# Performance work log

Hardware: AMD Instinct MI355X
Metric: run time of the kernel (lower is better)

## Reference

```python
import jax, jax.numpy as jnp
import numpy as np

N = 7          # N_AGENTS (hardcoded in source)
H = 4          # n_heads
TOP_K = 3
EPS = 1e-5
NEG = -1.0e9


def _gat(x, W, a_src, a_dst, edge_mask):
    # x: (B,N,F), W: (F,H*Hd), a_src/a_dst: (H,Hd), edge_mask: (N,N)
    B = x.shape[0]
    Hd = a_src.shape[1]
    h = (x @ W).reshape(B, N, H, Hd)
    s_src = jnp.einsum('bnhd,hd->bnh', h, a_src)
    s_dst = jnp.einsum('bnhd,hd->bnh', h, a_dst)
    e = s_src[:, :, None, :] + s_dst[:, None, :, :]          # (B,N,N,H)
    e = jnp.where(e > 0, e, 0.2 * e)                          # LeakyReLU(0.2)
    m = edge_mask[None, :, :, None]
    e = e * m + (1.0 - m) * NEG
    if TOP_K < N:
        # k-th largest along axis=2 (ascending sort -> index N-TOP_K)
        thr = jnp.sort(e, axis=2)[:, :, N - TOP_K:N - TOP_K + 1, :]
        sm = (e >= thr).astype(e.dtype)
        e = e * sm + (1.0 - sm) * NEG
    alpha = jax.nn.softmax(e, axis=2)
    alpha = jnp.nan_to_num(alpha)
    out = jnp.einsum('bijh,bjhd->bihd', alpha, h).reshape(B, N, H * Hd)
    return out, alpha.mean(-1)


def _ln(x, w, b):
    mu = x.mean(-1, keepdims=True)
    var = ((x - mu) ** 2).mean(-1, keepdims=True)
    return (x - mu) / jnp.sqrt(var + EPS) * w + b


def _forward(node_feats, context, base_preds, regime_feats, edge_logits,
             W1, a_src1, a_dst1, W2, a_src2, a_dst2,
             ln1_w, ln1_b, ln2_w, ln2_b, skip_w, skip_b,
             base_w1, base_b1, base_w2, base_b2,
             reg_w1, reg_b1, reg_w2, reg_b2,
             gate_w1, gate_b1, gate_w2, gate_b2,
             res_w1, res_b1, res_w2, res_b2):
    B = node_feats.shape[0]
    eye = jnp.eye(N, dtype=edge_logits.dtype)
    edge_mask = jax.nn.sigmoid(edge_logits) * (1.0 - eye) + eye

    skip = node_feats @ skip_w + skip_b
    h1, _ = _gat(node_feats, W1, a_src1, a_dst1, edge_mask)
    h = jax.nn.relu(_ln(h1 + skip, ln1_w, ln1_b))
    h2, attn = _gat(h, W2, a_src2, a_dst2, edge_mask)
    h = jax.nn.relu(_ln(h2 + h, ln2_w, ln2_b))

    combined = jnp.concatenate([h.reshape(B, -1), context], axis=-1)
    w_base = jax.nn.softmax(jax.nn.relu(combined @ base_w1 + base_b1) @ base_w2 + base_b2, axis=-1)
    w_regime = jax.nn.softmax(jax.nn.relu(combined @ reg_w1 + reg_b1) @ reg_w2 + reg_b2, axis=-1)
    gate = jax.nn.sigmoid(jnp.tanh(regime_feats @ gate_w1 + gate_b1) @ gate_w2 + gate_b2)  # (B,1)
    weights = (1.0 - gate) * w_base + gate * w_regime
    pred = (weights * base_preds).sum(-1)
    residual = (jnp.tanh(combined @ res_w1 + res_b1) @ res_w2 + res_b2)[:, 0] * 0.05
    pred = jnp.maximum(pred + residual, 0.05)
    return pred, weights, gate, edge_mask, attn


def setup_inputs() -> dict:
    key = jax.random.key(0)
    B, F, C, HID, NB = 16384, 256, 128, 256, 2
    Hd = HID // H
    G = N * HID + C
    ks = iter(jax.random.split(key, 40))
    nrm = lambda shp, s: jax.random.normal(next(ks), shp, jnp.float32) * s
    d = {
        'node_feats': nrm((B, N, F), 1.0),
        'context': nrm((B, C), 1.0),
        'base_preds': jax.random.uniform(next(ks), (B, NB), jnp.float32),
        'regime_feats': nrm((B, 3), 1.0),
        'edge_logits': nrm((N, N), 0.1),
        'W1': nrm((F, HID), (2.0 / (F + HID)) ** 0.5),
        'a_src1': nrm((H, Hd), 0.1), 'a_dst1': nrm((H, Hd), 0.1),
        'W2': nrm((HID, HID), (1.0 / HID) ** 0.5),
        'a_src2': nrm((H, Hd), 0.1), 'a_dst2': nrm((H, Hd), 0.1),
        'ln1_w': jnp.ones((HID,), jnp.float32), 'ln1_b': jnp.zeros((HID,), jnp.float32),
        'ln2_w': jnp.ones((HID,), jnp.float32), 'ln2_b': jnp.zeros((HID,), jnp.float32),
        'skip_w': nrm((F, HID), (1.0 / F) ** 0.5), 'skip_b': jnp.zeros((HID,), jnp.float32),
        'base_w1': nrm((G, 32), (1.0 / G) ** 0.5), 'base_b1': jnp.zeros((32,), jnp.float32),
        'base_w2': nrm((32, NB), 0.1), 'base_b2': jnp.zeros((NB,), jnp.float32),
        'reg_w1': nrm((G, 32), (1.0 / G) ** 0.5), 'reg_b1': jnp.zeros((32,), jnp.float32),
        'reg_w2': nrm((32, NB), 0.1), 'reg_b2': jnp.zeros((NB,), jnp.float32),
        'gate_w1': nrm((3, 8), 0.5), 'gate_b1': jnp.zeros((8,), jnp.float32),
        'gate_w2': nrm((8, 1), 0.3), 'gate_b2': jnp.zeros((1,), jnp.float32),
        'res_w1': nrm((G, 16), (1.0 / G) ** 0.5), 'res_b1': jnp.zeros((16,), jnp.float32),
        'res_w2': nrm((16, 1), 0.2), 'res_b2': jnp.zeros((1,), jnp.float32),
    }
    return d


def reference(node_feats, context, base_preds, regime_feats, edge_logits,
              W1, a_src1, a_dst1, W2, a_src2, a_dst2,
              ln1_w, ln1_b, ln2_w, ln2_b, skip_w, skip_b,
              base_w1, base_b1, base_w2, base_b2,
              reg_w1, reg_b1, reg_w2, reg_b2,
              gate_w1, gate_b1, gate_w2, gate_b2,
              res_w1, res_b1, res_w2, res_b2):
    return _forward(node_feats, context, base_preds, regime_feats, edge_logits,
                    W1, a_src1, a_dst1, W2, a_src2, a_dst2,
                    ln1_w, ln1_b, ln2_w, ln2_b, skip_w, skip_b,
                    base_w1, base_b1, base_w2, base_b2,
                    reg_w1, reg_b1, reg_w2, reg_b2,
                    gate_w1, gate_b1, gate_w2, gate_b2,
                    res_w1, res_b1, res_w2, res_b2)
```

## Files before the change

kernel.cpp:

```cpp
#include <hip/hip_runtime.h>
#include <hip/hip_bf16.h>

typedef unsigned short u16;
typedef __attribute__((ext_vector_type(8))) short bfrag8;
typedef __attribute__((ext_vector_type(8))) unsigned short u16x8;
typedef __attribute__((ext_vector_type(4))) unsigned short u16x4;
typedef __attribute__((ext_vector_type(4))) float f32x4;

__device__ __forceinline__ float bf2f(u16 u) {
    union { unsigned int i; float f; } v; v.i = ((unsigned int)u) << 16; return v.f;
}
__device__ __forceinline__ u16 f2bf(float f) {
    union { __hip_bfloat16 h; u16 u; } cv;
    cv.h = __float2bfloat16(f);
    return cv.u;
}
__device__ __forceinline__ float fast_tanh(float x) {
    float e = __expf(2.f * x);
    return (e - 1.f) / (e + 1.f);
}

#define TILE_M 128
#define TILE_N 128
#define TILE_K 32

#define GLOAD_LDS16(g, l) \
    __builtin_amdgcn_global_load_lds( \
        (const __attribute__((address_space(1))) void*)(g), \
        (__attribute__((address_space(3))) void*)(l), 16, 0, 0)

template<int HAS_BIAS, int C_MODE, int NGUARD>
__global__ __launch_bounds__(256)
void gemm_k(const u16* __restrict__ A, const u16* __restrict__ Bt,
            const float* __restrict__ bias, void* __restrict__ Cp,
            int M, int N, int K, int lda, int ldc, int nt, int kchunk)
{
    __shared__ u16 As[2][TILE_M][TILE_K];
    __shared__ u16 Bs[2][TILE_N][TILE_K];

    const int nwg = gridDim.x;
    const int q = nwg >> 3, r = nwg & 7;
    const int xcd = blockIdx.x & 7, pos = blockIdx.x >> 3;
    const int wg = (xcd < r ? xcd * (q + 1) : r * (q + 1) + (xcd - r) * q) + pos;
    const int m0 = (wg / nt) * TILE_M;
    const int n0 = (wg % nt) * TILE_N;

    const int kc   = blockIdx.y;
    const int kbeg = kc * kchunk;
    const int kend = (kbeg + kchunk < K) ? kbeg + kchunk : K;

    const int t    = threadIdx.x;
    const int lane = t & 63;
    const int w    = t >> 6;
    const int wm   = (w >> 1) * 64;
    const int wn   = (w & 1) * 64;
    const int lr   = lane & 15;
    const int kg   = (lane >> 4) * 8;

    const int lrow = lane >> 2;
    const int lcol = (lane & 3) * 8;
    const u16* gA0 = A  + (size_t)(m0 + 32 * w + lrow) * lda + lcol;
    const u16* gA1 = gA0 + (size_t)16 * lda;
    const u16* gB0 = Bt + (size_t)(n0 + 32 * w + lrow) * K + lcol;
    const u16* gB1 = gB0 + (size_t)16 * K;
    char* lA = (char*)&As[0][0][0] + w * 2048;
    char* lB = (char*)&Bs[0][0][0] + w * 2048;

    f32x4 acc[4][4];
#pragma unroll
    for (int i = 0; i < 4; ++i)
#pragma unroll
        for (int j = 0; j < 4; ++j) acc[i][j] = (f32x4){0.f, 0.f, 0.f, 0.f};

#define ISSUE(bufo, k0v) { \
        GLOAD_LDS16(gA0 + (k0v), lA + (bufo)); \
        GLOAD_LDS16(gA1 + (k0v), lA + 1024 + (bufo)); \
        GLOAD_LDS16(gB0 + (k0v), lB + (bufo)); \
        GLOAD_LDS16(gB1 + (k0v), lB + 1024 + (bufo)); \
    }

    ISSUE(0, kbeg)
    int buf = 0;
    for (int k0 = kbeg; k0 < kend; k0 += TILE_K) {
        const bool more = (k0 + TILE_K) < kend;
        if (more) {
            ISSUE((buf ^ 1) * 8192, k0 + TILE_K);
            asm volatile("s_waitcnt vmcnt(4)" ::: "memory");
        } else {
            asm volatile("s_waitcnt vmcnt(0)" ::: "memory");
        }
        __syncthreads();

        bfrag8 af[4], bfr[4];
#pragma unroll
        for (int mi = 0; mi < 4; ++mi) af[mi]  = *(const bfrag8*)&As[buf][wm + mi * 16 + lr][kg];
#pragma unroll
        for (int ni = 0; ni < 4; ++ni) bfr[ni] = *(const bfrag8*)&Bs[buf][wn + ni * 16 + lr][kg];
#pragma unroll
        for (int mi = 0; mi < 4; ++mi)
#pragma unroll
            for (int ni = 0; ni < 4; ++ni)
                acc[mi][ni] = __builtin_amdgcn_mfma_f32_16x16x32_bf16(af[mi], bfr[ni], acc[mi][ni], 0, 0, 0);

        __syncthreads();
        buf ^= 1;
    }
#undef ISSUE

    float* Cf = (float*)Cp + (size_t)kc * M * ldc;
#pragma unroll
    for (int mi = 0; mi < 4; ++mi) {
#pragma unroll
        for (int ni = 0; ni < 4; ++ni) {
            int col = n0 + wn + ni * 16 + lr;
            if (!NGUARD || col < N) {
                int row = m0 + wm + mi * 16 + (lane >> 4) * 4;
                float bv = 0.f;
                if (HAS_BIAS && kc == 0) bv = bias[col];
#pragma unroll
                for (int rr = 0; rr < 4; ++rr) {
                    float v = acc[mi][ni][rr] + bv;
                    if (C_MODE == 0) ((u16*)Cp)[(size_t)(row + rr) * ldc + col] = f2bf(v);
                    else             Cf[(size_t)(row + rr) * ldc + col] = v;
                }
            }
        }
    }
}

__global__ __launch_bounds__(256)
void precast_k(const float* __restrict__ in, u16* __restrict__ out, int n8)
{
    int i = blockIdx.x * 256 + threadIdx.x;
    if (i >= n8) return;
    const float4* p = (const float4*)(in + (size_t)i * 8);
    float4 a = p[0], b = p[1];
    u16x8 v;
    v[0] = f2bf(a.x); v[1] = f2bf(a.y); v[2] = f2bf(a.z); v[3] = f2bf(a.w);
    v[4] = f2bf(b.x); v[5] = f2bf(b.y); v[6] = f2bf(b.z); v[7] = f2bf(b.w);
    *(u16x8*)(out + (size_t)i * 8) = v;
}

__global__ __launch_bounds__(256)
void score_k(const u16* __restrict__ hs, int ld,
             const float* __restrict__ a_src, const float* __restrict__ a_dst,
             float* __restrict__ scores, int Mrows)
{
    const int wid  = blockIdx.x * 4 + (threadIdx.x >> 6);
    const int lane = threadIdx.x & 63;
    if (wid >= Mrows) return;
    const u16* hp = hs + (size_t)wid * ld + lane * 4;
    u16x4 xv = *(const u16x4*)hp;
    float s1 = 0.f, s2 = 0.f;
#pragma unroll
    for (int k = 0; k < 4; ++k) {
        float x = bf2f(xv[k]);
        s1 = fmaf(x, a_src[lane * 4 + k], s1);
        s2 = fmaf(x, a_dst[lane * 4 + k], s2);
    }
#pragma unroll
    for (int off = 1; off < 16; off <<= 1) {
        s1 += __shfl_xor(s1, off);
        s2 += __shfl_xor(s2, off);
    }
    if ((lane & 15) == 0) {
        scores[(size_t)wid * 8 + (lane >> 4)] = s1;
        scores[(size_t)wid * 8 + 4 + (lane >> 4)] = s2;
    }
}

template<int WRITE_ATTN>
__global__ __launch_bounds__(256)
void alpha_k(const float* __restrict__ scores, const float* __restrict__ em2,
             float* __restrict__ alpha, float* __restrict__ attn_out)
{
    const int t = blockIdx.x * 256 + threadIdx.x;
    const int b = t >> 2;
    const int h = t & 3;

    float ssrc[7], sdst[7];
#pragma unroll
    for (int n = 0; n < 7; ++n) {
        ssrc[n] = scores[(size_t)(b * 7 + n) * 8 + h];
        sdst[n] = scores[(size_t)(b * 7 + n) * 8 + 4 + h];
    }

    float al[49];
#pragma unroll
    for (int i = 0; i < 7; ++i) {
        float e[7];
#pragma unroll
        for (int j = 0; j < 7; ++j) {
            float v = ssrc[i] + sdst[j];
            v = fmaxf(v, 0.2f * v);
            e[j] = fmaf(v, em2[(i * 7 + j) * 2], em2[(i * 7 + j) * 2 + 1]);
        }
        float a1 = -3e38f, b1 = -3e38f, c1 = -3e38f;
#pragma unroll
        for (int j = 0; j < 7; ++j) {
            float v = e[j];
            float t2 = fminf(a1, v); a1 = fmaxf(a1, v);
            float t3 = fminf(b1, t2); b1 = fmaxf(b1, t2);
            c1 = fmaxf(c1, t3);
        }
        float psum = 0.f;
        float p[7];
#pragma unroll
        for (int j = 0; j < 7; ++j) {
            float qv = (e[j] >= c1) ? __expf(e[j] - a1) : 0.f;
            p[j] = qv; psum += qv;
        }
        float inv = 1.f / psum;
#pragma unroll
        for (int j = 0; j < 7; ++j) al[i * 7 + j] = p[j] * inv;
    }

    float* ap = alpha + (size_t)t * 49;
#pragma unroll
    for (int j = 0; j < 49; ++j) ap[j] = al[j];

    if (WRITE_ATTN) {
#pragma unroll
        for (int j = 0; j < 49; ++j) {
            float m = al[j];
            m += __shfl_xor(m, 1);
            m += __shfl_xor(m, 2);
            if (h == 0) attn_out[(size_t)b * 49 + j] = 0.25f * m;
        }
    }
}

__global__ __launch_bounds__(256)
void gat_apply_k(const u16* __restrict__ hh, int ld_hh,
                 const u16* __restrict__ resid, int ld_res, int res_off,
                 const float* __restrict__ alpha,
                 const float* __restrict__ ln_w, const float* __restrict__ ln_b,
                 u16* __restrict__ outp, int out_bs)
{
    const int t = threadIdx.x;
    const int b = blockIdx.x * 4 + (t >> 6);
    const int l = t & 63;
    const int c = l * 4;
    const int h = l >> 4;
    const size_t rowbase = (size_t)b * 7;

    float hv[7][4];
#pragma unroll
    for (int n = 0; n < 7; ++n) {
        u16x4 qv = *(const u16x4*)&hh[(rowbase + n) * ld_hh + c];
#pragma unroll
        for (int k = 0; k < 4; ++k) hv[n][k] = bf2f(qv[k]);
    }

    const float* ap = alpha + ((size_t)b * 4 + h) * 49;
    float4 lw = *(const float4*)&ln_w[c];
    float4 lb = *(const float4*)&ln_b[c];

#pragma unroll
    for (int i = 0; i < 7; ++i) {
        float a0 = ap[i * 7 + 0], a1 = ap[i * 7 + 1], a2 = ap[i * 7 + 2],
              a3 = ap[i * 7 + 3], a4 = ap[i * 7 + 4], a5 = ap[i * 7 + 5],
              a6 = ap[i * 7 + 6];
        u16x4 rr = *(const u16x4*)&resid[(rowbase + i) * ld_res + res_off + c];
        float x[4];
#pragma unroll
        for (int k = 0; k < 4; ++k) {
            float pv = a0 * hv[0][k];
            pv = fmaf(a1, hv[1][k], pv);
            pv = fmaf(a2, hv[2][k], pv);
            pv = fmaf(a3, hv[3][k], pv);
            pv = fmaf(a4, hv[4][k], pv);
            pv = fmaf(a5, hv[5][k], pv);
            pv = fmaf(a6, hv[6][k], pv);
            x[k] = pv + bf2f(rr[k]);
        }
        float s1 = (x[0] + x[1]) + (x[2] + x[3]);
        float s2 = fmaf(x[0], x[0], x[1] * x[1]) + fmaf(x[2], x[2], x[3] * x[3]);
#pragma unroll
        for (int off = 32; off > 0; off >>= 1) {
            s1 += __shfl_xor(s1, off);
            s2 += __shfl_xor(s2, off);
        }
        float mu  = s1 * (1.f / 256.f);
        float var = fmaxf(s2 * (1.f / 256.f) - mu * mu, 0.f);
        float inv = rsqrtf(var + 1e-5f);
        u16x4 o;
        o[0] = f2bf(fmaxf((x[0] - mu) * inv * lw.x + lb.x, 0.f));
        o[1] = f2bf(fmaxf((x[1] - mu) * inv * lw.y + lb.y, 0.f));
        o[2] = f2bf(fmaxf((x[2] - mu) * inv * lw.z + lb.z, 0.f));
        o[3] = f2bf(fmaxf((x[3] - mu) * inv * lw.w + lb.w, 0.f));
        *(u16x4*)&outp[(size_t)b * out_bs + i * 256 + c] = o;
    }
}

__global__ __launch_bounds__(256)
void prep_k(const float* __restrict__ W1, const float* __restrict__ skip_w, const float* __restrict__ W2,
            const float* __restrict__ base_w1, const float* __restrict__ reg_w1, const float* __restrict__ res_w1,
            const float* __restrict__ skip_b, const float* __restrict__ base_b1, const float* __restrict__ reg_b1,
            const float* __restrict__ res_b1, const float* __restrict__ edge_logits,
            u16* __restrict__ Wt1, u16* __restrict__ Wt2, u16* __restrict__ Wt3,
            float* __restrict__ bias1, float* __restrict__ bias3,
            float* __restrict__ em2, float* __restrict__ em_out)
{
    int idx = blockIdx.x * 256 + threadIdx.x;
    if (idx < 512 * 256) {
        int n = idx >> 8, k = idx & 255;
        float v = (n < 256) ? W1[k * 256 + n] : skip_w[k * 256 + (n - 256)];
        Wt1[n * 256 + k] = f2bf(v); return;
    }
    idx -= 512 * 256;
    if (idx < 256 * 256) {
        int n = idx >> 8, k = idx & 255;
        Wt2[n * 256 + k] = f2bf(W2[k * 256 + n]); return;
    }
    idx -= 256 * 256;
    if (idx < 128 * 1920) {
        int n = idx / 1920, k = idx % 1920;
        float v = (n < 32) ? base_w1[k * 32 + n]
                : (n < 64) ? reg_w1[k * 32 + (n - 32)]
                : (n < 80) ? res_w1[k * 16 + (n - 64)] : 0.f;
        Wt3[n * 1920 + k] = f2bf(v); return;
    }
    idx -= 128 * 1920;
    if (idx < 512) { bias1[idx] = (idx < 256) ? 0.f : skip_b[idx - 256]; return; }
    idx -= 512;
    if (idx < 80) {
        bias3[idx] = (idx < 32) ? base_b1[idx] : (idx < 64) ? reg_b1[idx - 32] : res_b1[idx - 64];
        return;
    }
    idx -= 80;
    if (idx < 49) {
        int i = idx / 7, j = idx % 7;
        float s = 1.f / (1.f + __expf(-edge_logits[idx]));
        float m = (i == j) ? 1.f : s;
        em2[idx * 2] = m;
        em2[idx * 2 + 1] = (1.f - m) * (-1e9f);
        em_out[idx] = m;
    }
}

__global__ __launch_bounds__(256)
void ctx_k(const float* __restrict__ ctx, u16* __restrict__ comb)
{
    int idx = blockIdx.x * 256 + threadIdx.x;
    int b = idx >> 7, cc = idx & 127;
    comb[(size_t)b * 1920 + 1792 + cc] = f2bf(ctx[idx]);
}

__global__ __launch_bounds__(64)
void head_finish(const float* __restrict__ ho,
                 const float* __restrict__ bp, const float* __restrict__ rf,
                 const float* __restrict__ bw2, const float* __restrict__ bb2,
                 const float* __restrict__ rw2, const float* __restrict__ rb2,
                 const float* __restrict__ gw1, const float* __restrict__ gb1,
                 const float* __restrict__ gw2, const float* __restrict__ gb2,
                 const float* __restrict__ resw2, const float* __restrict__ resb2,
                 float* __restrict__ out_pred, float* __restrict__ out_w, float* __restrict__ out_gate, int B)
{
    int b = blockIdx.x * 64 + threadIdx.x;
    if (b >= B) return;
    const size_t ss = (size_t)B * 80;
    const float* p = ho + (size_t)b * 80;

    float z0 = bb2[0], z1 = bb2[1];
#pragma unroll
    for (int j = 0; j < 32; j += 4) {
        float4 a0 = *(const float4*)(p + j);
        float4 a1 = *(const float4*)(p + ss + j);
        float4 a2 = *(const float4*)(p + 2 * ss + j);
        float4 a3 = *(const float4*)(p + 3 * ss + j);
        float v;
        v = fmaxf((a0.x + a1.x) + (a2.x + a3.x), 0.f); z0 = fmaf(v, bw2[2*j+0], z0); z1 = fmaf(v, bw2[2*j+1], z1);
        v = fmaxf((a0.y + a1.y) + (a2.y + a3.y), 0.f); z0 = fmaf(v, bw2[2*j+2], z0); z1 = fmaf(v, bw2[2*j+3], z1);
        v = fmaxf((a0.z + a1.z) + (a2.z + a3.z), 0.f); z0 = fmaf(v, bw2[2*j+4], z0); z1 = fmaf(v, bw2[2*j+5], z1);
        v = fmaxf((a0.w + a1.w) + (a2.w + a3.w), 0.f); z0 = fmaf(v, bw2[2*j+6], z0); z1 = fmaf(v, bw2[2*j+7], z1);
    }
    float mz = fmaxf(z0, z1); float e0 = __expf(z0 - mz), e1 = __expf(z1 - mz); float inv = 1.f / (e0 + e1);
    float wb0 = e0 * inv, wb1 = e1 * inv;

    z0 = rb2[0]; z1 = rb2[1];
#pragma unroll
    for (int j = 0; j < 32; j += 4) {
        float4 a0 = *(const float4*)(p + 32 + j);
        float4 a1 = *(const float4*)(p + ss + 32 + j);
        float4 a2 = *(const float4*)(p + 2 * ss + 32 + j);
        float4 a3 = *(const float4*)(p + 3 * ss + 32 + j);
        float v;
        v = fmaxf((a0.x + a1.x) + (a2.x + a3.x), 0.f); z0 = fmaf(v, rw2[2*j+0], z0); z1 = fmaf(v, rw2[2*j+1], z1);
        v = fmaxf((a0.y + a1.y) + (a2.y + a3.y), 0.f); z0 = fmaf(v, rw2[2*j+2], z0); z1 = fmaf(v, rw2[2*j+3], z1);
        v = fmaxf((a0.z + a1.z) + (a2.z + a3.z), 0.f); z0 = fmaf(v, rw2[2*j+4], z0); z1 = fmaf(v, rw2[2*j+5], z1);
        v = fmaxf((a0.w + a1.w) + (a2.w + a3.w), 0.f); z0 = fmaf(v, rw2[2*j+6], z0); z1 = fmaf(v, rw2[2*j+7], z1);
    }
    mz = fmaxf(z0, z1); e0 = __expf(z0 - mz); e1 = __expf(z1 - mz); inv = 1.f / (e0 + e1);
    float wr0 = e0 * inv, wr1 = e1 * inv;

    float r = resb2[0];
#pragma unroll
    for (int j = 0; j < 16; j += 4) {
        float4 a0 = *(const float4*)(p + 64 + j);
        float4 a1 = *(const float4*)(p + ss + 64 + j);
        float4 a2 = *(const float4*)(p + 2 * ss + 64 + j);
        float4 a3 = *(const float4*)(p + 3 * ss + 64 + j);
        r = fmaf(fast_tanh((a0.x + a1.x) + (a2.x + a3.x)), resw2[j + 0], r);
        r = fmaf(fast_tanh((a0.y + a1.y) + (a2.y + a3.y)), resw2[j + 1], r);
        r = fmaf(fast_tanh((a0.z + a1.z) + (a2.z + a3.z)), resw2[j + 2], r);
        r = fmaf(fast_tanh((a0.w + a1.w) + (a2.w + a3.w)), resw2[j + 3], r);
    }

    float g = gb2[0];
#pragma unroll
    for (int j = 0; j < 8; ++j) {
        float a = gb1[j];
#pragma unroll
        for (int i = 0; i < 3; ++i) a += rf[(size_t)b * 3 + i] * gw1[i * 8 + j];
        g += fast_tanh(a) * gw2[j];
    }
    float gg = 1.f / (1.f + __expf(-g));
    float w0 = (1.f - gg) * wb0 + gg * wr0;
    float w1 = (1.f - gg) * wb1 + gg * wr1;
    float pred = w0 * bp[(size_t)b * 2] + w1 * bp[(size_t)b * 2 + 1];
    pred = fmaxf(pred + r * 0.05f, 0.05f);
    out_pred[b] = pred;
    out_w[(size_t)b * 2] = w0; out_w[(size_t)b * 2 + 1] = w1;
    out_gate[b] = gg;
}

extern "C" void kernel_launch(void* const* d_in, const int* in_sizes, int n_in,
                              void* d_out, int out_size, void* d_ws, size_t ws_size,
                              hipStream_t stream)
{
    const int B = in_sizes[1] / 128;
    const int Mbig = B * 7;

    const float* node_feats   = (const float*)d_in[0];
    const float* context      = (const float*)d_in[1];
    const float* base_preds   = (const float*)d_in[2];
    const float* regime_feats = (const float*)d_in[3];
    const float* edge_logits  = (const float*)d_in[4];
    const float* W1      = (const float*)d_in[5];
    const float* a_src1  = (const float*)d_in[6];
    const float* a_dst1  = (const float*)d_in[7];
    const float* W2      = (const float*)d_in[8];
    const float* a_src2  = (const float*)d_in[9];
    const float* a_dst2  = (const float*)d_in[10];
    const float* ln1_w   = (const float*)d_in[11];
    const float* ln1_b   = (const float*)d_in[12];
    const float* ln2_w   = (const float*)d_in[13];
    const float* ln2_b   = (const float*)d_in[14];
    const float* skip_w  = (const float*)d_in[15];
    const float* skip_b  = (const float*)d_in[16];
    const float* base_w1 = (const float*)d_in[17];
    const float* base_b1 = (const float*)d_in[18];
    const float* base_w2 = (const float*)d_in[19];
    const float* base_b2 = (const float*)d_in[20];
    const float* reg_w1  = (const float*)d_in[21];
    const float* reg_b1  = (const float*)d_in[22];
    const float* reg_w2  = (const float*)d_in[23];
    const float* reg_b2  = (const float*)d_in[24];
    const float* gate_w1 = (const float*)d_in[25];
    const float* gate_b1 = (const float*)d_in[26];
    const float* gate_w2 = (const float*)d_in[27];
    const float* gate_b2 = (const float*)d_in[28];
    const float* res_w1  = (const float*)d_in[29];
    const float* res_b1  = (const float*)d_in[30];
    const float* res_w2  = (const float*)d_in[31];
    const float* res_b2  = (const float*)d_in[32];

    char* ws = (char*)d_ws;
    size_t off = 0;
    u16* hs1 = (u16*)(ws + off);
    u16* hh2 = (u16*)(ws + off);
    off += (size_t)Mbig * 512 * 2;
    u16* hbuf = (u16*)(ws + off);  off += (size_t)Mbig * 256 * 2;
    u16* comb = (u16*)(ws + off);  off += (size_t)B * 1920 * 2;
    u16* nf_bf = comb;
    float* headout = (float*)(ws + off); off += (size_t)4 * B * 80 * 4;
    u16* Wt1 = (u16*)(ws + off); off += 512 * 256 * 2;
    u16* Wt2 = (u16*)(ws + off); off += 256 * 256 * 2;
    u16* Wt3 = (u16*)(ws + off); off += (size_t)128 * 1920 * 2;
    float* bias1 = (float*)(ws + off); off += 512 * 4;
    float* bias3 = (float*)(ws + off); off += 128 * 4;
    float* em2   = (float*)(ws + off); off += 128 * 4;
    float* scoresb = (float*)(ws + off); off += (size_t)Mbig * 8 * 4;
    float* alphab  = (float*)(ws + off); off += (size_t)B * 4 * 49 * 4;

    float* out_pred = (float*)d_out;
    float* out_w    = out_pred + B;
    float* out_gate = out_pred + 3 * (size_t)B;
    float* out_em   = out_pred + 4 * (size_t)B;
    float* out_attn = out_pred + 4 * (size_t)B + 49;

    const int B4blocks = (B * 4) / 256;

    {
        int n8 = Mbig * 256 / 8;
        precast_k<<<dim3((n8 + 255) / 256), dim3(256), 0, stream>>>(node_feats, nf_bf, n8);
    }

    prep_k<<<dim3(1731), dim3(256), 0, stream>>>(W1, skip_w, W2, base_w1, reg_w1, res_w1,
        skip_b, base_b1, reg_b1, res_b1, edge_logits, Wt1, Wt2, Wt3, bias1, bias3, em2, out_em);

    gemm_k<1, 0, 0><<<dim3((Mbig / 128) * 4, 1), dim3(256), 0, stream>>>(
        nf_bf, Wt1, bias1, (void*)hs1, Mbig, 512, 256, 256, 512, 4, 256);

    score_k<<<dim3(Mbig / 4), dim3(256), 0, stream>>>(hs1, 512, a_src1, a_dst1, scoresb, Mbig);

    alpha_k<0><<<dim3(B4blocks), dim3(256), 0, stream>>>(scoresb, em2, alphab, (float*)nullptr);

    gat_apply_k<<<dim3(B / 4), dim3(256), 0, stream>>>(
        hs1, 512, hs1, 512, 256, alphab, ln1_w, ln1_b, hbuf, 1792);

    gemm_k<0, 0, 0><<<dim3((Mbig / 128) * 2, 1), dim3(256), 0, stream>>>(
        hbuf, Wt2, (const float*)nullptr, (void*)hh2, Mbig, 256, 256, 256, 256, 2, 256);

    score_k<<<dim3(Mbig / 4), dim3(256), 0, stream>>>(hh2, 256, a_src2, a_dst2, scoresb, Mbig);

    alpha_k<1><<<dim3(B4blocks), dim3(256), 0, stream>>>(scoresb, em2, alphab, out_attn);

    gat_apply_k<<<dim3(B / 4), dim3(256), 0, stream>>>(
        hh2, 256, hbuf, 256, 0, alphab, ln2_w, ln2_b, comb, 1920);

    ctx_k<<<dim3(B * 128 / 256), dim3(256), 0, stream>>>(context, comb);

    gemm_k<1, 1, 1><<<dim3(B / 128, 4), dim3(256), 0, stream>>>(
        comb, Wt3, bias3, (void*)headout, B, 80, 1920, 1920, 80, 1, 480);

    head_finish<<<dim3((B + 63) / 64), dim3(64), 0, stream>>>(
        headout, base_preds, regime_feats, base_w2, base_b2, reg_w2, reg_b2,
        gate_w1, gate_b1, gate_w2, gate_b2, res_w2, res_b2, out_pred, out_w, out_gate, B);
}
```

Measured before the change: 289.1 us.

## Replace double-buffered GEMM K loop with single-buffer templated BK tile

```diff
diff --git a/kernel.cpp b/kernel.cpp
--- a/kernel.cpp
+++ b/kernel.cpp
@@ -22,21 +22,20 @@
 
 #define TILE_M 128
 #define TILE_N 128
-#define TILE_K 32
 
 #define GLOAD_LDS16(g, l) \
     __builtin_amdgcn_global_load_lds( \
         (const __attribute__((address_space(1))) void*)(g), \
         (__attribute__((address_space(3))) void*)(l), 16, 0, 0)
 
-template<int HAS_BIAS, int C_MODE, int NGUARD>
+template<int BK, int HAS_BIAS, int C_MODE, int NGUARD>
 __global__ __launch_bounds__(256)
 void gemm_k(const u16* __restrict__ A, const u16* __restrict__ Bt,
             const float* __restrict__ bias, void* __restrict__ Cp,
             int M, int N, int K, int lda, int ldc, int nt, int kchunk)
 {
-    __shared__ u16 As[2][TILE_M][TILE_K];
-    __shared__ u16 Bs[2][TILE_N][TILE_K];
+    __shared__ u16 As[TILE_M][BK];
+    __shared__ u16 Bs[TILE_N][BK];
 
     const int nwg = gridDim.x;
     const int q = nwg >> 3, r = nwg & 7;
@@ -57,14 +56,15 @@
     const int lr   = lane & 15;
     const int kg   = (lane >> 4) * 8;
 
-    const int lrow = lane >> 2;
-    const int lcol = (lane & 3) * 8;
-    const u16* gA0 = A  + (size_t)(m0 + 32 * w + lrow) * lda + lcol;
-    const u16* gA1 = gA0 + (size_t)16 * lda;
-    const u16* gB0 = Bt + (size_t)(n0 + 32 * w + lrow) * K + lcol;
-    const u16* gB1 = gB0 + (size_t)16 * K;
-    char* lA = (char*)&As[0][0][0] + w * 2048;
-    char* lB = (char*)&Bs[0][0][0] + w * 2048;
+    constexpr int ISSUES = BK / 16;
+
+    int irow[ISSUES], icol[ISSUES];
+#pragma unroll
+    for (int j = 0; j < ISSUES; ++j) {
+        int off = j * 4096 + t * 16;
+        irow[j] = off / (2 * BK);
+        icol[j] = (off & (2 * BK - 1)) >> 1;
+    }
 
     f32x4 acc[4][4];
 #pragma unroll
@@ -72,40 +72,33 @@
 #pragma unroll
         for (int j = 0; j < 4; ++j) acc[i][j] = (f32x4){0.f, 0.f, 0.f, 0.f};
 
-#define ISSUE(bufo, k0v) { \
-        GLOAD_LDS16(gA0 + (k0v), lA + (bufo)); \
-        GLOAD_LDS16(gA1 + (k0v), lA + 1024 + (bufo)); \
-        GLOAD_LDS16(gB0 + (k0v), lB + (bufo)); \
-        GLOAD_LDS16(gB1 + (k0v), lB + 1024 + (bufo)); \
-    }
-
-    ISSUE(0, kbeg)
-    int buf = 0;
-    for (int k0 = kbeg; k0 < kend; k0 += TILE_K) {
-        const bool more = (k0 + TILE_K) < kend;
-        if (more) {
-            ISSUE((buf ^ 1) * 8192, k0 + TILE_K);
-            asm volatile("s_waitcnt vmcnt(4)" ::: "memory");
-        } else {
-            asm volatile("s_waitcnt vmcnt(0)" ::: "memory");
-        }
+    char* lA = (char*)&As[0][0];
+    char* lB = (char*)&Bs[0][0];
+
+    for (int k0 = kbeg; k0 < kend; k0 += BK) {
+#pragma unroll
+        for (int j = 0; j < ISSUES; ++j) {
+            GLOAD_LDS16(A  + (size_t)(m0 + irow[j]) * lda + k0 + icol[j], lA + j * 4096 + t * 16);
+            GLOAD_LDS16(Bt + (size_t)(n0 + irow[j]) * K   + k0 + icol[j], lB + j * 4096 + t * 16);
+        }
+        asm volatile("s_waitcnt vmcnt(0)" ::: "memory");
         __syncthreads();
 
-        bfrag8 af[4], bfr[4];
-#pragma unroll
-        for (int mi = 0; mi < 4; ++mi) af[mi]  = *(const bfrag8*)&As[buf][wm + mi * 16 + lr][kg];
-#pragma unroll
-        for (int ni = 0; ni < 4; ++ni) bfr[ni] = *(const bfrag8*)&Bs[buf][wn + ni * 16 + lr][kg];
-#pragma unroll
-        for (int mi = 0; mi < 4; ++mi)
-#pragma unroll
-            for (int ni = 0; ni < 4; ++ni)
-                acc[mi][ni] = __builtin_amdgcn_mfma_f32_16x16x32_bf16(af[mi], bfr[ni], acc[mi][ni], 0, 0, 0);
-
+#pragma unroll
+        for (int ks = 0; ks < BK / 32; ++ks) {
+            bfrag8 af[4], bfr[4];
+#pragma unroll
+            for (int mi = 0; mi < 4; ++mi) af[mi]  = *(const bfrag8*)&As[wm + mi * 16 + lr][ks * 32 + kg];
+#pragma unroll
+            for (int ni = 0; ni < 4; ++ni) bfr[ni] = *(const bfrag8*)&Bs[wn + ni * 16 + lr][ks * 32 + kg];
+#pragma unroll
+            for (int mi = 0; mi < 4; ++mi)
+#pragma unroll
+                for (int ni = 0; ni < 4; ++ni)
+                    acc[mi][ni] = __builtin_amdgcn_mfma_f32_16x16x32_bf16(af[mi], bfr[ni], acc[mi][ni], 0, 0, 0);
+        }
         __syncthreads();
-        buf ^= 1;
-    }
-#undef ISSUE
+    }
 
     float* Cf = (float*)Cp + (size_t)kc * M * ldc;
 #pragma unroll
@@ -500,7 +493,7 @@
     prep_k<<<dim3(1731), dim3(256), 0, stream>>>(W1, skip_w, W2, base_w1, reg_w1, res_w1,
         skip_b, base_b1, reg_b1, res_b1, edge_logits, Wt1, Wt2, Wt3, bias1, bias3, em2, out_em);
 
-    gemm_k<1, 0, 0><<<dim3((Mbig / 128) * 4, 1), dim3(256), 0, stream>>>(
+    gemm_k<64, 1, 0, 0><<<dim3((Mbig / 128) * 4, 1), dim3(256), 0, stream>>>(
         nf_bf, Wt1, bias1, (void*)hs1, Mbig, 512, 256, 256, 512, 4, 256);
 
     score_k<<<dim3(Mbig / 4), dim3(256), 0, stream>>>(hs1, 512, a_src1, a_dst1, scoresb, Mbig);
@@ -510,7 +503,7 @@
     gat_apply_k<<<dim3(B / 4), dim3(256), 0, stream>>>(
         hs1, 512, hs1, 512, 256, alphab, ln1_w, ln1_b, hbuf, 1792);
 
-    gemm_k<0, 0, 0><<<dim3((Mbig / 128) * 2, 1), dim3(256), 0, stream>>>(
+    gemm_k<64, 0, 0, 0><<<dim3((Mbig / 128) * 2, 1), dim3(256), 0, stream>>>(
         hbuf, Wt2, (const float*)nullptr, (void*)hh2, Mbig, 256, 256, 256, 256, 2, 256);
 
     score_k<<<dim3(Mbig / 4), dim3(256), 0, stream>>>(hh2, 256, a_src2, a_dst2, scoresb, Mbig);
@@ -522,7 +515,7 @@
 
     ctx_k<<<dim3(B * 128 / 256), dim3(256), 0, stream>>>(context, comb);
 
-    gemm_k<1, 1, 1><<<dim3(B / 128, 4), dim3(256), 0, stream>>>(
+    gemm_k<32, 1, 1, 1><<<dim3(B / 128, 4), dim3(256), 0, stream>>>(
         comb, Wt3, bias3, (void*)headout, B, 80, 1920, 1920, 80, 1, 480);
 
     head_finish<<<dim3((B + 63) / 64), dim3(64), 0, stream>>>(
```

Result: slower. 309.1 us (+6.9%).

## Fuse GAT attention score computation into GEMM epilogue and single-buffer LDS

Applied to the files above, without the earlier changes.

```diff
diff --git a/kernel.cpp b/kernel.cpp
--- a/kernel.cpp
+++ b/kernel.cpp
@@ -29,14 +29,16 @@
         (const __attribute__((address_space(1))) void*)(g), \
         (__attribute__((address_space(3))) void*)(l), 16, 0, 0)
 
-template<int HAS_BIAS, int C_MODE, int NGUARD>
+template<int HAS_BIAS, int C_MODE, int NGUARD, int SCORES>
 __global__ __launch_bounds__(256)
 void gemm_k(const u16* __restrict__ A, const u16* __restrict__ Bt,
             const float* __restrict__ bias, void* __restrict__ Cp,
-            int M, int N, int K, int lda, int ldc, int nt, int kchunk)
-{
-    __shared__ u16 As[2][TILE_M][TILE_K];
-    __shared__ u16 Bs[2][TILE_N][TILE_K];
+            int M, int N, int K, int lda, int ldc, int nt, int kchunk,
+            const float* __restrict__ a_src, const float* __restrict__ a_dst,
+            float* __restrict__ scores, int ns)
+{
+    __shared__ u16 As[TILE_M][TILE_K];
+    __shared__ u16 Bs[TILE_N][TILE_K];
 
     const int nwg = gridDim.x;
     const int q = nwg >> 3, r = nwg & 7;
@@ -63,8 +65,10 @@
     const u16* gA1 = gA0 + (size_t)16 * lda;
     const u16* gB0 = Bt + (size_t)(n0 + 32 * w + lrow) * K + lcol;
     const u16* gB1 = gB0 + (size_t)16 * K;
-    char* lA = (char*)&As[0][0][0] + w * 2048;
-    char* lB = (char*)&Bs[0][0][0] + w * 2048;
+    char* lA0 = (char*)&As[0][0] + w * 2048;
+    char* lA1 = lA0 + 1024;
+    char* lB0 = (char*)&Bs[0][0] + w * 2048;
+    char* lB1 = lB0 + 1024;
 
     f32x4 acc[4][4];
 #pragma unroll
@@ -72,30 +76,19 @@
 #pragma unroll
         for (int j = 0; j < 4; ++j) acc[i][j] = (f32x4){0.f, 0.f, 0.f, 0.f};
 
-#define ISSUE(bufo, k0v) { \
-        GLOAD_LDS16(gA0 + (k0v), lA + (bufo)); \
-        GLOAD_LDS16(gA1 + (k0v), lA + 1024 + (bufo)); \
-        GLOAD_LDS16(gB0 + (k0v), lB + (bufo)); \
-        GLOAD_LDS16(gB1 + (k0v), lB + 1024 + (bufo)); \
-    }
-
-    ISSUE(0, kbeg)
-    int buf = 0;
     for (int k0 = kbeg; k0 < kend; k0 += TILE_K) {
-        const bool more = (k0 + TILE_K) < kend;
-        if (more) {
-            ISSUE((buf ^ 1) * 8192, k0 + TILE_K);
-            asm volatile("s_waitcnt vmcnt(4)" ::: "memory");
-        } else {
-            asm volatile("s_waitcnt vmcnt(0)" ::: "memory");
-        }
+        GLOAD_LDS16(gA0 + k0, lA0);
+        GLOAD_LDS16(gA1 + k0, lA1);
+        GLOAD_LDS16(gB0 + k0, lB0);
+        GLOAD_LDS16(gB1 + k0, lB1);
+        asm volatile("s_waitcnt vmcnt(0)" ::: "memory");
         __syncthreads();
 
         bfrag8 af[4], bfr[4];
 #pragma unroll
-        for (int mi = 0; mi < 4; ++mi) af[mi]  = *(const bfrag8*)&As[buf][wm + mi * 16 + lr][kg];
-#pragma unroll
-        for (int ni = 0; ni < 4; ++ni) bfr[ni] = *(const bfrag8*)&Bs[buf][wn + ni * 16 + lr][kg];
+        for (int mi = 0; mi < 4; ++mi) af[mi]  = *(const bfrag8*)&As[wm + mi * 16 + lr][kg];
+#pragma unroll
+        for (int ni = 0; ni < 4; ++ni) bfr[ni] = *(const bfrag8*)&Bs[wn + ni * 16 + lr][kg];
 #pragma unroll
         for (int mi = 0; mi < 4; ++mi)
 #pragma unroll
@@ -103,9 +96,7 @@
                 acc[mi][ni] = __builtin_amdgcn_mfma_f32_16x16x32_bf16(af[mi], bfr[ni], acc[mi][ni], 0, 0, 0);
 
         __syncthreads();
-        buf ^= 1;
-    }
-#undef ISSUE
+    }
 
     float* Cf = (float*)Cp + (size_t)kc * M * ldc;
 #pragma unroll
@@ -122,6 +113,39 @@
                     float v = acc[mi][ni][rr] + bv;
                     if (C_MODE == 0) ((u16*)Cp)[(size_t)(row + rr) * ldc + col] = f2bf(v);
                     else             Cf[(size_t)(row + rr) * ldc + col] = v;
+                }
+            }
+        }
+    }
+
+    if (SCORES && n0 < ns) {
+        const int h = (n0 + wn) >> 6;
+        float as[4], ad[4];
+#pragma unroll
+        for (int ni = 0; ni < 4; ++ni) {
+            int col = n0 + wn + ni * 16 + lr;
+            as[ni] = a_src[col]; ad[ni] = a_dst[col];
+        }
+#pragma unroll
+        for (int mi = 0; mi < 4; ++mi) {
+#pragma unroll
+            for (int rr = 0; rr < 4; ++rr) {
+                float p1 = 0.f, p2 = 0.f;
+#pragma unroll
+                for (int ni = 0; ni < 4; ++ni) {
+                    float v = acc[mi][ni][rr];
+                    p1 = fmaf(v, as[ni], p1);
+                    p2 = fmaf(v, ad[ni], p2);
+                }
+#pragma unroll
+                for (int o = 1; o < 16; o <<= 1) {
+                    p1 += __shfl_xor(p1, o);
+                    p2 += __shfl_xor(p2, o);
+                }
+                if (lr == 0) {
+                    int row = m0 + wm + mi * 16 + (lane >> 4) * 4 + rr;
+                    scores[(size_t)row * 8 + h] = p1;
+                    scores[(size_t)row * 8 + 4 + h] = p2;
                 }
             }
         }
@@ -139,34 +163,6 @@
     v[0] = f2bf(a.x); v[1] = f2bf(a.y); v[2] = f2bf(a.z); v[3] = f2bf(a.w);
     v[4] = f2bf(b.x); v[5] = f2bf(b.y); v[6] = f2bf(b.z); v[7] = f2bf(b.w);
     *(u16x8*)(out + (size_t)i * 8) = v;
-}
-
-__global__ __launch_bounds__(256)
-void score_k(const u16* __restrict__ hs, int ld,
-             const float* __restrict__ a_src, const float* __restrict__ a_dst,
-             float* __restrict__ scores, int Mrows)
-{
-    const int wid  = blockIdx.x * 4 + (threadIdx.x >> 6);
-    const int lane = threadIdx.x & 63;
-    if (wid >= Mrows) return;
-    const u16* hp = hs + (size_t)wid * ld + lane * 4;
-    u16x4 xv = *(const u16x4*)hp;
-    float s1 = 0.f, s2 = 0.f;
-#pragma unroll
-    for (int k = 0; k < 4; ++k) {
-        float x = bf2f(xv[k]);
-        s1 = fmaf(x, a_src[lane * 4 + k], s1);
-        s2 = fmaf(x, a_dst[lane * 4 + k], s2);
-    }
-#pragma unroll
-    for (int off = 1; off < 16; off <<= 1) {
-        s1 += __shfl_xor(s1, off);
-        s2 += __shfl_xor(s2, off);
-    }
-    if ((lane & 15) == 0) {
-        scores[(size_t)wid * 8 + (lane >> 4)] = s1;
-        scores[(size_t)wid * 8 + 4 + (lane >> 4)] = s2;
-    }
 }
 
 template<int WRITE_ATTN>
@@ -500,20 +496,18 @@
     prep_k<<<dim3(1731), dim3(256), 0, stream>>>(W1, skip_w, W2, base_w1, reg_w1, res_w1,
         skip_b, base_b1, reg_b1, res_b1, edge_logits, Wt1, Wt2, Wt3, bias1, bias3, em2, out_em);
 
-    gemm_k<1, 0, 0><<<dim3((Mbig / 128) * 4, 1), dim3(256), 0, stream>>>(
-        nf_bf, Wt1, bias1, (void*)hs1, Mbig, 512, 256, 256, 512, 4, 256);
-
-    score_k<<<dim3(Mbig / 4), dim3(256), 0, stream>>>(hs1, 512, a_src1, a_dst1, scoresb, Mbig);
+    gemm_k<1, 0, 0, 1><<<dim3((Mbig / 128) * 4, 1), dim3(256), 0, stream>>>(
+        nf_bf, Wt1, bias1, (void*)hs1, Mbig, 512, 256, 256, 512, 4, 256,
+        a_src1, a_dst1, scoresb, 256);
 
     alpha_k<0><<<dim3(B4blocks), dim3(256), 0, stream>>>(scoresb, em2, alphab, (float*)nullptr);
 
     gat_apply_k<<<dim3(B / 4), dim3(256), 0, stream>>>(
         hs1, 512, hs1, 512, 256, alphab, ln1_w, ln1_b, hbuf, 1792);
 
-    gemm_k<0, 0, 0><<<dim3((Mbig / 128) * 2, 1), dim3(256), 0, stream>>>(
-        hbuf, Wt2, (const float*)nullptr, (void*)hh2, Mbig, 256, 256, 256, 256, 2, 256);
-
-    score_k<<<dim3(Mbig / 4), dim3(256), 0, stream>>>(hh2, 256, a_src2, a_dst2, scoresb, Mbig);
+    gemm_k<0, 0, 0, 1><<<dim3((Mbig / 128) * 2, 1), dim3(256), 0, stream>>>(
+        hbuf, Wt2, (const float*)nullptr, (void*)hh2, Mbig, 256, 256, 256, 256, 2, 256,
+        a_src2, a_dst2, scoresb, 256);
 
     alpha_k<1><<<dim3(B4blocks), dim3(256), 0, stream>>>(scoresb, em2, alphab, out_attn);
 
@@ -522,8 +516,9 @@
 
     ctx_k<<<dim3(B * 128 / 256), dim3(256), 0, stream>>>(context, comb);
 
-    gemm_k<1, 1, 1><<<dim3(B / 128, 4), dim3(256), 0, stream>>>(
-        comb, Wt3, bias3, (void*)headout, B, 80, 1920, 1920, 80, 1, 480);
+    gemm_k<1, 1, 1, 0><<<dim3(B / 128, 4), dim3(256), 0, stream>>>(
+        comb, Wt3, bias3, (void*)headout, B, 80, 1920, 1920, 80, 1, 480,
+        (const float*)nullptr, (const float*)nullptr, (float*)nullptr, 0);
 
     head_finish<<<dim3((B + 63) / 64), dim3(64), 0, stream>>>(
         headout, base_preds, regime_feats, base_w2, base_b2, reg_w2, reg_b2,
```

Result: no change. 284.3 us (-1.7%).
